# Performance work log

Measured on AMD Instinct MI355X. Metric: run time of the kernel, lower is better.

The kernel has to match this reference:

```python
import jax, jax.numpy as jnp
import numpy as np

B, P, F = 128, 196, 2048   # batch, num_pixels, feature_dim
E, H, V = 512, 512, 10000  # embed_dim, hidden_dim, vocab_size
T = 32                     # max caption length


def setup_inputs() -> dict:
    key = jax.random.key(0)
    ks = jax.random.split(key, 12)
    s_e, s_h, s_f = 1.0 / np.sqrt(E), 1.0 / np.sqrt(H), 1.0 / np.sqrt(F)
    return {
        "features": jax.random.normal(ks[0], (B, P, F), jnp.float32),
        "captions": jax.random.randint(ks[1], (B, T), 0, V),
        # embedding table (init uniform(-0.1, 0.1) in the original)
        "emb_W": jax.random.uniform(ks[2], (V, E), jnp.float32, -0.1, 0.1),
        # LSTMCell params (PyTorch layout: [4H, in] with gate order i,f,g,o)
        "W_ih": jax.random.uniform(ks[3], (4 * H, E), jnp.float32, -s_h, s_h),
        "W_hh": jax.random.uniform(ks[4], (4 * H, H), jnp.float32, -s_h, s_h),
        "b_ih": jax.random.uniform(ks[5], (4 * H,), jnp.float32, -s_h, s_h),
        "b_hh": jax.random.uniform(ks[6], (4 * H,), jnp.float32, -s_h, s_h),
        # init_h / init_c linear layers: feature_dim -> hidden_dim
        "Wh": jax.random.uniform(ks[7], (H, F), jnp.float32, -s_f, s_f),
        "bh": jax.random.uniform(ks[8], (H,), jnp.float32, -s_f, s_f),
        "Wc": jax.random.uniform(ks[9], (H, F), jnp.float32, -s_f, s_f),
        "bc": jax.random.uniform(ks[10], (H,), jnp.float32, -s_f, s_f),
        # output projection (uniform(-0.1, 0.1) weights, zero bias)
        "fc_W": jax.random.uniform(ks[11], (V, H), jnp.float32, -0.1, 0.1),
        "fc_b": jnp.zeros((V,), jnp.float32),
    }


def _decode(features, captions, emb_W, W_ih, W_hh, b_ih, b_hh, Wh, bh, Wc, bc, fc_W, fc_b):
    # init hidden state from mean pooled features
    mean_feat = features.mean(axis=1)                       # [B, F]
    h0 = mean_feat @ Wh.T + bh                              # [B, H]
    c0 = mean_feat @ Wc.T + bc                              # [B, H]

    embeds = emb_W[captions]                                # [B, T, E]
    # x-side gate preactivations for all steps at once: [T-1, B, 4H]
    x_gates = jnp.einsum('bte,ge->tbg', embeds[:, :-1, :], W_ih) + (b_ih + b_hh)

    def step(carry, xg):
        h, c = carry
        gates = xg + h @ W_hh.T                             # [B, 4H]
        i, f, g, o = jnp.split(gates, 4, axis=-1)
        i, f, o = jax.nn.sigmoid(i), jax.nn.sigmoid(f), jax.nn.sigmoid(o)
        g = jnp.tanh(g)
        c_new = f * c + i * g
        h_new = o * jnp.tanh(c_new)
        return (h_new, c_new), h_new

    _, hs = jax.lax.scan(step, (h0, c0), x_gates)           # hs: [T-1, B, H]
    hs = jnp.swapaxes(hs, 0, 1)                             # [B, T-1, H]
    # dropout is identity in eval mode; fc applied per step == batched matmul
    return jnp.einsum('bth,vh->btv', hs, fc_W) + fc_b       # [B, T-1, V]


def reference(features, captions, emb_W, W_ih, W_hh, b_ih, b_hh, Wh, bh, Wc, bc, fc_W, fc_b):
    return _decode(features, captions, emb_W, W_ih, W_hh, b_ih, b_hh, Wh, bh, Wc, bc, fc_W, fc_b)
```

## Files before the change

kernel.cpp:

```cpp
#include <hip/hip_runtime.h>
#include <hip/hip_bf16.h>
#include <cstddef>

#define Bz 128
#define Pz 196
#define Fz 2048
#define Ez 512
#define Hz 512
#define Vz 10000
#define Tz 32
#define TM 31
#define Mrows (Bz * TM)
#define MPAD 4096
#define G4 (4 * Hz)
#define NPAD 10240

typedef __attribute__((ext_vector_type(8))) short bf16x8;
typedef __attribute__((ext_vector_type(4))) float f32x4;

__device__ __forceinline__ void gload_lds16(const void* g, void* l) {
    __builtin_amdgcn_global_load_lds(
        (const __attribute__((address_space(1))) unsigned int*)g,
        (__attribute__((address_space(3))) unsigned int*)l, 16, 0, 0);
}
__device__ __forceinline__ ushort f2b(float x) {
    __hip_bfloat16 b = __float2bfloat16(x);
    return *reinterpret_cast<ushort*>(&b);
}
__device__ __forceinline__ float b2f(ushort u) {
    __hip_bfloat16 b = *reinterpret_cast<__hip_bfloat16*>(&u);
    return __bfloat162float(b);
}

__global__ __launch_bounds__(256) void meanpool(const float* __restrict__ feat,
                                                float* __restrict__ mean) {
    int idx = blockIdx.x * 256 + threadIdx.x;
    int b = idx >> 9;
    int q = idx & 511;
    const float4* base = reinterpret_cast<const float4*>(feat) +
                         (size_t)b * Pz * (Fz / 4) + q;
    float4 acc = {0.f, 0.f, 0.f, 0.f};
    for (int p = 0; p < Pz; ++p) {
        float4 v = base[(size_t)p * (Fz / 4)];
        acc.x += v.x; acc.y += v.y; acc.z += v.z; acc.w += v.w;
    }
    const float s = 1.0f / (float)Pz;
    acc.x *= s; acc.y *= s; acc.z *= s; acc.w *= s;
    reinterpret_cast<float4*>(mean)[idx] = acc;
}

__global__ __launch_bounds__(256) void gather_cvt_emb(const float* __restrict__ emb,
                                                      const int* __restrict__ cap,
                                                      ushort* __restrict__ out) {
    int idx = blockIdx.x * 256 + threadIdx.x;
    if (idx >= Mrows * (Ez / 4)) return;
    int m = idx >> 7, kq = idx & 127;
    int b = m / TM;
    int t = m - b * TM;
    int row = cap[b * Tz + t];
    float4 v = reinterpret_cast<const float4*>(emb + (size_t)row * Ez)[kq];
    ushort4 o = {f2b(v.x), f2b(v.y), f2b(v.z), f2b(v.w)};
    reinterpret_cast<ushort4*>(out + (size_t)m * Ez)[kq] = o;
}

__global__ __launch_bounds__(256) void permute_w(
    const float* __restrict__ Wih, const float* __restrict__ Whh,
    const float* __restrict__ b1,  const float* __restrict__ b2,
    ushort* __restrict__ WihP, ushort* __restrict__ WhhP,
    float* __restrict__ bP) {
    int idx = blockIdx.x * 256 + threadIdx.x;
    int sel = idx >> 18;
    int rem = idx & ((1 << 18) - 1);
    int o = rem >> 7, kq = rem & 127;
    int j = o >> 2, g = o & 3;
    int in = g * Hz + j;
    if (sel == 0) {
        float4 v = reinterpret_cast<const float4*>(Wih + (size_t)in * Ez)[kq];
        ushort4 u = {f2b(v.x), f2b(v.y), f2b(v.z), f2b(v.w)};
        reinterpret_cast<ushort4*>(WihP + (size_t)o * Ez)[kq] = u;
        if (kq == 0) bP[o] = b1[in] + b2[in];
    } else {
        float4 v = reinterpret_cast<const float4*>(Whh + (size_t)in * Hz)[kq];
        ushort4 u = {f2b(v.x), f2b(v.y), f2b(v.z), f2b(v.w)};
        reinterpret_cast<ushort4*>(WhhP + (size_t)o * Hz)[kq] = u;
    }
}

__global__ __launch_bounds__(256) void cvt_bf16_pad4(const float* __restrict__ s,
                                                     ushort* __restrict__ d,
                                                     int n4src, int n4dst) {
    int i = blockIdx.x * 256 + threadIdx.x;
    if (i >= n4dst) return;
    ushort4 o;
    if (i < n4src) {
        float4 v = reinterpret_cast<const float4*>(s)[i];
        o.x = f2b(v.x); o.y = f2b(v.y); o.z = f2b(v.z); o.w = f2b(v.w);
    } else {
        o.x = o.y = o.z = o.w = 0;
    }
    reinterpret_cast<ushort4*>(d)[i] = o;
}

__global__ __launch_bounds__(256) void initk(
    const float* __restrict__ mean,
    const float* __restrict__ Wh, const float* __restrict__ Wc,
    float* __restrict__ partial)
{
    __shared__ float As[64][33];
    __shared__ float Bs2[64][33];
    const int n0 = blockIdx.x * 64;
    const int m0 = blockIdx.y * 64;
    const int kz = blockIdx.z;
    const int tid = threadIdx.x;
    const int tx = tid & 15, ty = tid >> 4;
    float acc[4][4] = {};

    for (int k0 = kz * 256; k0 < kz * 256 + 256; k0 += 32) {
#pragma unroll
        for (int i = 0; i < 2; ++i) {
            int e  = tid + i * 256;
            int r  = e >> 3;
            int cc = (e & 7) << 2;
            float4 va = *reinterpret_cast<const float4*>(
                mean + (size_t)(m0 + r) * Fz + k0 + cc);
            As[r][cc + 0] = va.x; As[r][cc + 1] = va.y;
            As[r][cc + 2] = va.z; As[r][cc + 3] = va.w;
            int n = n0 + r;
            const float* Brow = (n < Hz) ? (Wh + (size_t)n * Fz)
                                         : (Wc + (size_t)(n - Hz) * Fz);
            float4 vb = *reinterpret_cast<const float4*>(Brow + k0 + cc);
            Bs2[r][cc + 0] = vb.x; Bs2[r][cc + 1] = vb.y;
            Bs2[r][cc + 2] = vb.z; Bs2[r][cc + 3] = vb.w;
        }
        __syncthreads();
#pragma unroll
        for (int kk = 0; kk < 32; ++kk) {
            float a[4], bb[4];
#pragma unroll
            for (int i = 0; i < 4; ++i) a[i] = As[ty * 4 + i][kk];
#pragma unroll
            for (int j = 0; j < 4; ++j) bb[j] = Bs2[tx * 4 + j][kk];
#pragma unroll
            for (int i = 0; i < 4; ++i)
#pragma unroll
                for (int j = 0; j < 4; ++j)
                    acc[i][j] += a[i] * bb[j];
        }
        __syncthreads();
    }
#pragma unroll
    for (int i = 0; i < 4; ++i)
#pragma unroll
        for (int j = 0; j < 4; ++j)
            partial[((size_t)kz * 128 + m0 + ty * 4 + i) * 1024 + n0 + tx * 4 + j]
                = acc[i][j];
}

__global__ __launch_bounds__(256) void init_reduce(
    const float* __restrict__ partial,
    const float* __restrict__ bh, const float* __restrict__ bc,
    ushort* __restrict__ haHi, ushort* __restrict__ haLo,
    float* __restrict__ c0f)
{
    int idx = blockIdx.x * 256 + threadIdx.x;
    if (idx >= 128 * 1024) return;
    int m = idx >> 10, n = idx & 1023;
    float s = 0.f;
#pragma unroll
    for (int z = 0; z < 8; ++z)
        s += partial[((size_t)z * 128 + m) * 1024 + n];
    if (n < Hz) {
        s += bh[n];
        ushort hh = f2b(s);
        haHi[(size_t)m * Hz + n] = hh;
        haLo[(size_t)m * Hz + n] = f2b(s - b2f(hh));
    } else {
        c0f[(size_t)m * Hz + (n - Hz)] = s + bc[n - Hz];
    }
}

__global__ __launch_bounds__(256) void gemm_mfma(
    const ushort* __restrict__ A,
    const ushort* __restrict__ B,
    const float* __restrict__ bias,
    float* __restrict__ C,
    int Nb, int ldc, int K)
{
    __shared__ short Al[2][128 * 32];
    __shared__ short Bl[2][128 * 32];
    const int tid  = threadIdx.x;
    const int w    = tid >> 6;
    const int lane = tid & 63;

    const int nwg  = gridDim.x * gridDim.y;
    int orig = blockIdx.y * gridDim.x + blockIdx.x;
    int q = nwg >> 3, r = nwg & 7;
    int xcd = orig & 7, local = orig >> 3;
    int wgid = (xcd < r ? xcd * (q + 1) : r * (q + 1) + (xcd - r) * q) + local;
    const int m0 = (wgid / gridDim.x) * 128;
    const int n0 = (wgid % gridDim.x) * 128;
    const int wr = w >> 1, wc = w & 1;

    f32x4 acc[4][4] = {};

    const int srow = w * 32 + (lane >> 2);
    const int scol = (lane & 3) * 16;
    const char* Ag = (const char*)(A + (size_t)(m0 + srow) * K) + scol;
    const char* Bg = (const char*)(B + (size_t)(n0 + srow) * K) + scol;
    const size_t rstep = (size_t)16 * K * 2;
    const int ldsb = (w * 32) * 32;

    const int ko = (lane >> 4) * 8;
    const int fr = lane & 15;
    const int nk = K >> 5;

    gload_lds16(Ag,         Al[0] + ldsb);
    gload_lds16(Ag + rstep, Al[0] + ldsb + 16 * 32);
    gload_lds16(Bg,         Bl[0] + ldsb);
    gload_lds16(Bg + rstep, Bl[0] + ldsb + 16 * 32);
    __syncthreads();

    int cur = 0;
    for (int k = 0; k < nk; ++k) {
        if (k + 1 < nk) {
            const size_t kb = (size_t)(k + 1) * 64;
            gload_lds16(Ag + kb,         Al[cur ^ 1] + ldsb);
            gload_lds16(Ag + kb + rstep, Al[cur ^ 1] + ldsb + 16 * 32);
            gload_lds16(Bg + kb,         Bl[cur ^ 1] + ldsb);
            gload_lds16(Bg + kb + rstep, Bl[cur ^ 1] + ldsb + 16 * 32);
        }
        bf16x8 af[4], bf[4];
#pragma unroll
        for (int i = 0; i < 4; ++i)
            af[i] = *reinterpret_cast<const bf16x8*>(&Al[cur][(wr * 64 + i * 16 + fr) * 32 + ko]);
#pragma unroll
        for (int j = 0; j < 4; ++j)
            bf[j] = *reinterpret_cast<const bf16x8*>(&Bl[cur][(wc * 64 + j * 16 + fr) * 32 + ko]);
#pragma unroll
        for (int i = 0; i < 4; ++i)
#pragma unroll
            for (int j = 0; j < 4; ++j)
                acc[i][j] = __builtin_amdgcn_mfma_f32_16x16x32_bf16(
                    af[i], bf[j], acc[i][j], 0, 0, 0);
        __syncthreads();
        cur ^= 1;
    }

    const int r0 = (lane >> 4) * 4;
#pragma unroll
    for (int i = 0; i < 4; ++i) {
        int row = m0 + wr * 64 + i * 16 + r0;
#pragma unroll
        for (int j = 0; j < 4; ++j) {
            int col = n0 + wc * 64 + j * 16 + fr;
            if (col < Nb) {
                float bb = bias ? bias[col] : 0.f;
#pragma unroll
                for (int rr = 0; rr < 4; ++rr)
                    C[(size_t)(row + rr) * ldc + col] = acc[i][j][rr] + bb;
            }
        }
    }
}

__global__ __launch_bounds__(512) void fc256(
    const ushort* __restrict__ A,
    const ushort* __restrict__ B,
    const float* __restrict__ bias,
    float* __restrict__ C)
{
    __shared__ short Al[2][256 * 32];
    __shared__ short Bl[2][256 * 32];
    const int tid  = threadIdx.x;
    const int w    = tid >> 6;
    const int lane = tid & 63;

    int orig = blockIdx.x;
    int wgid = (orig & 7) * 80 + (orig >> 3);
    const int m0 = (wgid / 40) * 256;
    const int n0 = (wgid % 40) * 256;
    const int wr = w >> 2, wc = w & 3;

    f32x4 acc[8][4] = {};

    const int srow = w * 32 + (lane >> 2);
    const int scol = (lane & 3) * 16;
    const char* Ag = (const char*)(A + (size_t)(m0 + srow) * Hz) + scol;
    const char* Bg = (const char*)(B + (size_t)(n0 + srow) * Hz) + scol;
    const size_t rstep = (size_t)16 * Hz * 2;
    const int ldsb = (w * 32) * 32;

    const int ko = (lane >> 4) * 8;
    const int fr = lane & 15;

    gload_lds16(Ag,         Al[0] + ldsb);
    gload_lds16(Ag + rstep, Al[0] + ldsb + 16 * 32);
    gload_lds16(Bg,         Bl[0] + ldsb);
    gload_lds16(Bg + rstep, Bl[0] + ldsb + 16 * 32);
    __syncthreads();

    int cur = 0;
#pragma unroll 1
    for (int k = 0; k < 16; ++k) {
        if (k < 15) {
            const size_t kb = (size_t)(k + 1) * 64;
            gload_lds16(Ag + kb,         Al[cur ^ 1] + ldsb);
            gload_lds16(Ag + kb + rstep, Al[cur ^ 1] + ldsb + 16 * 32);
            gload_lds16(Bg + kb,         Bl[cur ^ 1] + ldsb);
            gload_lds16(Bg + kb + rstep, Bl[cur ^ 1] + ldsb + 16 * 32);
        }
        bf16x8 bf[4];
#pragma unroll
        for (int j = 0; j < 4; ++j)
            bf[j] = *reinterpret_cast<const bf16x8*>(&Bl[cur][(wc * 64 + j * 16 + fr) * 32 + ko]);
#pragma unroll
        for (int i = 0; i < 8; ++i) {
            bf16x8 af = *reinterpret_cast<const bf16x8*>(&Al[cur][(wr * 128 + i * 16 + fr) * 32 + ko]);
#pragma unroll
            for (int j = 0; j < 4; ++j)
                acc[i][j] = __builtin_amdgcn_mfma_f32_16x16x32_bf16(
                    af, bf[j], acc[i][j], 0, 0, 0);
        }
        __syncthreads();
        cur ^= 1;
    }

    const int r0 = (lane >> 4) * 4;
#pragma unroll
    for (int i = 0; i < 8; ++i) {
        int row = m0 + wr * 128 + i * 16 + r0;
        if (row >= Mrows) continue;
#pragma unroll
        for (int j = 0; j < 4; ++j) {
            int col = n0 + wc * 64 + j * 16 + fr;
            if (col < Vz) {
                float bb = bias[col];
#pragma unroll
                for (int rr = 0; rr < 4; ++rr)
                    C[(size_t)(row + rr) * Vz + col] = acc[i][j][rr] + bb;
            }
        }
    }
}

__global__ __launch_bounds__(256) void lstm_step3(
    const float* __restrict__ xg,
    const ushort* __restrict__ Whi,
    const ushort* __restrict__ Ah,  const ushort* __restrict__ Alo,
    ushort* __restrict__ Oh, ushort* __restrict__ Ol,
    float* __restrict__ cst, ushort* __restrict__ hsb, int t)
{
    __shared__ float Cl[2][32][33];

    const int tid  = threadIdx.x;
    const int w    = tid >> 6;
    const int kh   = w >> 1;
    const int ch   = w & 1;
    const int lane = tid & 63;
    const int fr   = lane & 15;
    const int hi4  = lane >> 4;
    const int n0   = blockIdx.x * 32;
    const int j0   = blockIdx.x * 8;
    const int m0w  = blockIdx.y * 32;

    const int lm = tid >> 3;
    const int hq = tid & 7;
    const int em = m0w + lm;
    const int ej = j0 + hq;
    const float4 xv = *reinterpret_cast<const float4*>(
        xg + ((size_t)em * TM + t) * G4 + n0 + hq * 4);
    const float cold = cst[(size_t)em * Hz + ej];

    f32x4 acc[2] = {};
    const size_t kbase = (size_t)kh * 256;
    const ushort* Bp  = Whi + (size_t)(n0 + ch * 16 + fr) * Hz + kbase;
    const ushort* Ap0 = Ah  + (size_t)(m0w + fr) * Hz + kbase;
    const ushort* Ap1 = Ah  + (size_t)(m0w + 16 + fr) * Hz + kbase;
    const ushort* Lp0 = Alo + (size_t)(m0w + fr) * Hz + kbase;
    const ushort* Lp1 = Alo + (size_t)(m0w + 16 + fr) * Hz + kbase;

#pragma unroll
    for (int kc = 0; kc < 8; ++kc) {
        const size_t koff = (size_t)kc * 32 + hi4 * 8;
        bf16x8 bv  = *reinterpret_cast<const bf16x8*>(Bp  + koff);
        bf16x8 ah0 = *reinterpret_cast<const bf16x8*>(Ap0 + koff);
        bf16x8 ah1 = *reinterpret_cast<const bf16x8*>(Ap1 + koff);
        bf16x8 al0 = *reinterpret_cast<const bf16x8*>(Lp0 + koff);
        bf16x8 al1 = *reinterpret_cast<const bf16x8*>(Lp1 + koff);
        acc[0] = __builtin_amdgcn_mfma_f32_16x16x32_bf16(ah0, bv, acc[0], 0, 0, 0);
        acc[1] = __builtin_amdgcn_mfma_f32_16x16x32_bf16(ah1, bv, acc[1], 0, 0, 0);
        acc[0] = __builtin_amdgcn_mfma_f32_16x16x32_bf16(al0, bv, acc[0], 0, 0, 0);
        acc[1] = __builtin_amdgcn_mfma_f32_16x16x32_bf16(al1, bv, acc[1], 0, 0, 0);
    }

#pragma unroll
    for (int i = 0; i < 2; ++i)
#pragma unroll
        for (int r = 0; r < 4; ++r)
            Cl[kh][i * 16 + hi4 * 4 + r][ch * 16 + fr] = acc[i][r];
    __syncthreads();

    {
        const int bc = hq * 4;
        float gi = Cl[0][lm][bc + 0] + Cl[1][lm][bc + 0] + xv.x;
        float gf = Cl[0][lm][bc + 1] + Cl[1][lm][bc + 1] + xv.y;
        float gg = Cl[0][lm][bc + 2] + Cl[1][lm][bc + 2] + xv.z;
        float go = Cl[0][lm][bc + 3] + Cl[1][lm][bc + 3] + xv.w;

        float ig = 1.f / (1.f + expf(-gi));
        float fg = 1.f / (1.f + expf(-gf));
        float gt = tanhf(gg);
        float og = 1.f / (1.f + expf(-go));

        float cn = fg * cold + ig * gt;
        float hv = og * tanhf(cn);
        cst[(size_t)em * Hz + ej] = cn;

        ushort hh = f2b(hv);
        ushort hl = f2b(hv - b2f(hh));
        Oh[(size_t)em * Hz + ej] = hh;
        Ol[(size_t)em * Hz + ej] = hl;
        hsb[((size_t)em * TM + t) * Hz + ej] = hh;
    }
}

extern "C" void kernel_launch(void* const* d_in, const int* in_sizes, int n_in,
                              void* d_out, int out_size, void* d_ws, size_t ws_size,
                              hipStream_t stream) {
    const float* features = (const float*)d_in[0];
    const int*   captions = (const int*)d_in[1];
    const float* emb_W    = (const float*)d_in[2];
    const float* W_ih     = (const float*)d_in[3];
    const float* W_hh     = (const float*)d_in[4];
    const float* b_ih     = (const float*)d_in[5];
    const float* b_hh     = (const float*)d_in[6];
    const float* Wh       = (const float*)d_in[7];
    const float* bh       = (const float*)d_in[8];
    const float* Wc       = (const float*)d_in[9];
    const float* bc       = (const float*)d_in[10];
    const float* fc_W     = (const float*)d_in[11];
    const float* fc_b     = (const float*)d_in[12];
    float* out = (float*)d_out;

    float* w    = (float*)d_ws;
    float* mean = w;
    float* xg   = mean + Bz * Fz;
    float* partial = xg;
    float* c0f  = xg + (size_t)Mrows * G4;
    float* bP   = c0f + Bz * Hz;
    ushort* embg = (ushort*)(bP + G4);
    ushort* WihP = embg + (size_t)Mrows * Ez;
    ushort* Whi  = WihP + (size_t)G4 * Ez;
    ushort* fcWb = Whi + (size_t)G4 * Hz;
    ushort* hsb  = fcWb + (size_t)NPAD * Hz;
    ushort* haHi = hsb + (size_t)MPAD * Hz;
    ushort* haLo = haHi + Bz * Hz;
    ushort* hbHi = haLo + Bz * Hz;
    ushort* hbLo = hbHi + Bz * Hz;

    meanpool<<<(Bz * Fz / 4) / 256, 256, 0, stream>>>(features, mean);
    gather_cvt_emb<<<(Mrows * (Ez / 4) + 255) / 256, 256, 0, stream>>>(emb_W, captions, embg);
    permute_w<<<(2 * G4 * (Hz / 4)) / 256, 256, 0, stream>>>(
        W_ih, W_hh, b_ih, b_hh, WihP, Whi, bP);
    cvt_bf16_pad4<<<(NPAD * Hz / 4 + 255) / 256, 256, 0, stream>>>(
        fc_W, fcWb, Vz * Hz / 4, NPAD * Hz / 4);

    initk<<<dim3(16, 2, 8), 256, 0, stream>>>(mean, Wh, Wc, partial);
    init_reduce<<<(128 * 1024) / 256, 256, 0, stream>>>(
        partial, bh, bc, haHi, haLo, c0f);

    gemm_mfma<<<dim3(G4 / 128, Mrows / 128), 256, 0, stream>>>(
        embg, WihP, bP, xg, G4, G4, Ez);

    for (int t = 0; t < TM; ++t) {
        const ushort* ih = (t & 1) ? hbHi : haHi;
        const ushort* il = (t & 1) ? hbLo : haLo;
        ushort* oh = (t & 1) ? haHi : hbHi;
        ushort* ol = (t & 1) ? haLo : hbLo;
        lstm_step3<<<dim3(64, 4), 256, 0, stream>>>(
            xg, Whi, ih, il, oh, ol, c0f, hsb, t);
    }

    fc256<<<640, 512, 0, stream>>>(hsb, fcWb, fc_b, out);
}
```

Baseline: 436.7 us.

## Deepen FC GEMM pipeline to four LDS stages with swizzled layout

Rewrites the output-projection GEMM main loop to use a 4-buffer LDS ring with three stages of global-to-LDS loads in flight, using explicit vmcnt waits instead of a full __syncthreads per iteration. It also XOR-swizzles the LDS layout to reduce bank conflicts on fragment reads, preloads all A/B fragments before the MFMA block, and raises wave priority during MFMAs. This is meant to hide global memory latency and LDS conflicts better, at the cost of 128KB of LDS, which limits occupancy to one block per CU.

```diff
diff --git a/kernel.cpp b/kernel.cpp
--- a/kernel.cpp
+++ b/kernel.cpp
@@ -263,17 +263,18 @@
     }
 }
 
-__global__ __launch_bounds__(512) void fc256(
+__global__ __launch_bounds__(512) void fc8(
     const ushort* __restrict__ A,
     const ushort* __restrict__ B,
     const float* __restrict__ bias,
     float* __restrict__ C)
 {
-    __shared__ short Al[2][256 * 32];
-    __shared__ short Bl[2][256 * 32];
+    __shared__ short Lds[4][2][256 * 32];
+
     const int tid  = threadIdx.x;
     const int w    = tid >> 6;
     const int lane = tid & 63;
+    const int fr   = lane & 15;
 
     int orig = blockIdx.x;
     int wgid = (orig & 7) * 80 + (orig >> 3);
@@ -283,47 +284,69 @@
 
     f32x4 acc[8][4] = {};
 
-    const int srow = w * 32 + (lane >> 2);
-    const int scol = (lane & 3) * 16;
-    const char* Ag = (const char*)(A + (size_t)(m0 + srow) * Hz) + scol;
-    const char* Bg = (const char*)(B + (size_t)(n0 + srow) * Hz) + scol;
-    const size_t rstep = (size_t)16 * Hz * 2;
-    const int ldsb = (w * 32) * 32;
-
-    const int ko = (lane >> 4) * 8;
-    const int fr = lane & 15;
-
-    gload_lds16(Ag,         Al[0] + ldsb);
-    gload_lds16(Ag + rstep, Al[0] + ldsb + 16 * 32);
-    gload_lds16(Bg,         Bl[0] + ldsb);
-    gload_lds16(Bg + rstep, Bl[0] + ldsb + 16 * 32);
-    __syncthreads();
-
-    int cur = 0;
+    const int sw16 = (((lane & 3) ^ ((lane >> 3) & 3)) << 4);
+    const int srowA = lane >> 2;
+
+    const int rsw = (((lane >> 4) ^ ((fr >> 1) & 3)) << 4);
+
+#define FC_STAGE(T_) do {                                                     \
+    const int b_ = (T_) & 3;                                                  \
+    const size_t kb_ = (size_t)(T_) * 64;                                     \
+    _Pragma("unroll")                                                         \
+    for (int q_ = 0; q_ < 2; ++q_) {                                          \
+        const int R_ = w * 32 + q_ * 16;                                      \
+        gload_lds16((const char*)A + (size_t)(m0 + R_ + srowA) * 1024 + kb_ + sw16, \
+                    (char*)&Lds[b_][0][0] + R_ * 64);                         \
+        gload_lds16((const char*)B + (size_t)(n0 + R_ + srowA) * 1024 + kb_ + sw16, \
+                    (char*)&Lds[b_][1][0] + R_ * 64);                         \
+    }                                                                         \
+} while (0)
+
+#define FC_ITER(K_, VM_) do {                                                 \
+    if ((K_) + 3 <= 15) FC_STAGE((K_) + 3);                                   \
+    asm volatile("s_waitcnt vmcnt(" #VM_ ")" ::: "memory");                   \
+    __builtin_amdgcn_s_barrier();                                             \
+    __builtin_amdgcn_sched_barrier(0);                                        \
+    const int b_ = (K_) & 3;                                                  \
+    const char* Ab_ = (const char*)&Lds[b_][0][0];                            \
+    const char* Bb_ = (const char*)&Lds[b_][1][0];                            \
+    bf16x8 bfr_[4];                                                           \
+    _Pragma("unroll")                                                         \
+    for (int j_ = 0; j_ < 4; ++j_)                                            \
+        bfr_[j_] = *reinterpret_cast<const bf16x8*>(                          \
+            Bb_ + (wc * 64 + j_ * 16 + fr) * 64 + rsw);                       \
+    bf16x8 afr_[8];                                                           \
+    _Pragma("unroll")                                                         \
+    for (int i_ = 0; i_ < 8; ++i_)                                            \
+        afr_[i_] = *reinterpret_cast<const bf16x8*>(                          \
+            Ab_ + (wr * 128 + i_ * 16 + fr) * 64 + rsw);                      \
+    asm volatile("s_waitcnt lgkmcnt(0)" ::: "memory");                        \
+    __builtin_amdgcn_sched_barrier(0);                                        \
+    __builtin_amdgcn_s_barrier();                                             \
+    __builtin_amdgcn_s_setprio(1);                                            \
+    _Pragma("unroll")                                                         \
+    for (int i_ = 0; i_ < 8; ++i_)                                            \
+        _Pragma("unroll")                                                     \
+        for (int j_ = 0; j_ < 4; ++j_)                                        \
+            acc[i_][j_] = __builtin_amdgcn_mfma_f32_16x16x32_bf16(            \
+                afr_[i_], bfr_[j_], acc[i_][j_], 0, 0, 0);                    \
+    __builtin_amdgcn_s_setprio(0);                                            \
+} while (0)
+
+    FC_STAGE(0);
+    FC_STAGE(1);
+    FC_STAGE(2);
+
 #pragma unroll 1
-    for (int k = 0; k < 16; ++k) {
-        if (k < 15) {
-            const size_t kb = (size_t)(k + 1) * 64;
-            gload_lds16(Ag + kb,         Al[cur ^ 1] + ldsb);
-            gload_lds16(Ag + kb + rstep, Al[cur ^ 1] + ldsb + 16 * 32);
-            gload_lds16(Bg + kb,         Bl[cur ^ 1] + ldsb);
-            gload_lds16(Bg + kb + rstep, Bl[cur ^ 1] + ldsb + 16 * 32);
-        }
-        bf16x8 bf[4];
-#pragma unroll
-        for (int j = 0; j < 4; ++j)
-            bf[j] = *reinterpret_cast<const bf16x8*>(&Bl[cur][(wc * 64 + j * 16 + fr) * 32 + ko]);
-#pragma unroll
-        for (int i = 0; i < 8; ++i) {
-            bf16x8 af = *reinterpret_cast<const bf16x8*>(&Al[cur][(wr * 128 + i * 16 + fr) * 32 + ko]);
-#pragma unroll
-            for (int j = 0; j < 4; ++j)
-                acc[i][j] = __builtin_amdgcn_mfma_f32_16x16x32_bf16(
-                    af, bf[j], acc[i][j], 0, 0, 0);
-        }
-        __syncthreads();
-        cur ^= 1;
-    }
+    for (int k = 0; k <= 12; ++k) {
+        FC_ITER(k, 12);
+    }
+    FC_ITER(13, 8);
+    FC_ITER(14, 4);
+    FC_ITER(15, 0);
+
+#undef FC_STAGE
+#undef FC_ITER
 
     const int r0 = (lane >> 4) * 4;
 #pragma unroll
@@ -481,5 +504,5 @@
             xg, Whi, ih, il, oh, ol, c0f, hsb, t);
     }
 
-    fc256<<<640, 512, 0, stream>>>(hsb, fcWb, fc_b, out);
-}
+    fc8<<<640, 512, 0, stream>>>(hsb, fcWb, fc_b, out);
+}
```

Result: no change. 428.9 us (-1.8%).

## Overlap FC projection of previous step with LSTM recurrence in fused kernel

Applied to the files above, without the earlier changes.

Removes the separate large fc256 GEMM and instead has each per-timestep launch carry 64 extra blocks that compute the vocabulary projection for the previous step's hidden states. The launch loop runs one extra iteration to finish the last step. This aims to fill idle CUs during the latency-bound recurrence with the output GEMM. In exchange the FC work loses LDS tiling and reads fc_W directly from global memory every step, which puts more bandwidth pressure on the recurrent critical path.

```diff
diff --git a/kernel.cpp b/kernel.cpp
--- a/kernel.cpp
+++ b/kernel.cpp
@@ -263,105 +263,73 @@
     }
 }
 
-__global__ __launch_bounds__(512) void fc256(
-    const ushort* __restrict__ A,
-    const ushort* __restrict__ B,
-    const float* __restrict__ bias,
-    float* __restrict__ C)
-{
-    __shared__ short Al[2][256 * 32];
-    __shared__ short Bl[2][256 * 32];
-    const int tid  = threadIdx.x;
-    const int w    = tid >> 6;
-    const int lane = tid & 63;
-
-    int orig = blockIdx.x;
-    int wgid = (orig & 7) * 80 + (orig >> 3);
-    const int m0 = (wgid / 40) * 256;
-    const int n0 = (wgid % 40) * 256;
-    const int wr = w >> 2, wc = w & 3;
-
-    f32x4 acc[8][4] = {};
-
-    const int srow = w * 32 + (lane >> 2);
-    const int scol = (lane & 3) * 16;
-    const char* Ag = (const char*)(A + (size_t)(m0 + srow) * Hz) + scol;
-    const char* Bg = (const char*)(B + (size_t)(n0 + srow) * Hz) + scol;
-    const size_t rstep = (size_t)16 * Hz * 2;
-    const int ldsb = (w * 32) * 32;
-
-    const int ko = (lane >> 4) * 8;
-    const int fr = lane & 15;
-
-    gload_lds16(Ag,         Al[0] + ldsb);
-    gload_lds16(Ag + rstep, Al[0] + ldsb + 16 * 32);
-    gload_lds16(Bg,         Bl[0] + ldsb);
-    gload_lds16(Bg + rstep, Bl[0] + ldsb + 16 * 32);
-    __syncthreads();
-
-    int cur = 0;
-#pragma unroll 1
-    for (int k = 0; k < 16; ++k) {
-        if (k < 15) {
-            const size_t kb = (size_t)(k + 1) * 64;
-            gload_lds16(Ag + kb,         Al[cur ^ 1] + ldsb);
-            gload_lds16(Ag + kb + rstep, Al[cur ^ 1] + ldsb + 16 * 32);
-            gload_lds16(Bg + kb,         Bl[cur ^ 1] + ldsb);
-            gload_lds16(Bg + kb + rstep, Bl[cur ^ 1] + ldsb + 16 * 32);
-        }
-        bf16x8 bf[4];
-#pragma unroll
-        for (int j = 0; j < 4; ++j)
-            bf[j] = *reinterpret_cast<const bf16x8*>(&Bl[cur][(wc * 64 + j * 16 + fr) * 32 + ko]);
-#pragma unroll
-        for (int i = 0; i < 8; ++i) {
-            bf16x8 af = *reinterpret_cast<const bf16x8*>(&Al[cur][(wr * 128 + i * 16 + fr) * 32 + ko]);
-#pragma unroll
-            for (int j = 0; j < 4; ++j)
-                acc[i][j] = __builtin_amdgcn_mfma_f32_16x16x32_bf16(
-                    af, bf[j], acc[i][j], 0, 0, 0);
-        }
-        __syncthreads();
-        cur ^= 1;
-    }
-
-    const int r0 = (lane >> 4) * 4;
-#pragma unroll
-    for (int i = 0; i < 8; ++i) {
-        int row = m0 + wr * 128 + i * 16 + r0;
-        if (row >= Mrows) continue;
-#pragma unroll
-        for (int j = 0; j < 4; ++j) {
-            int col = n0 + wc * 64 + j * 16 + fr;
-            if (col < Vz) {
-                float bb = bias[col];
-#pragma unroll
-                for (int rr = 0; rr < 4; ++rr)
-                    C[(size_t)(row + rr) * Vz + col] = acc[i][j][rr] + bb;
-            }
-        }
-    }
-}
-
-__global__ __launch_bounds__(256) void lstm_step3(
+__global__ __launch_bounds__(256) void lstm_fused(
     const float* __restrict__ xg,
     const ushort* __restrict__ Whi,
     const ushort* __restrict__ Ah,  const ushort* __restrict__ Alo,
     ushort* __restrict__ Oh, ushort* __restrict__ Ol,
-    float* __restrict__ cst, ushort* __restrict__ hsb, int t)
+    float* __restrict__ cst, ushort* __restrict__ hsb,
+    const ushort* __restrict__ fcWb, const float* __restrict__ fc_b,
+    float* __restrict__ out, int t)
 {
-    __shared__ float Cl[2][32][33];
-
+    const int beta = blockIdx.x;
     const int tid  = threadIdx.x;
-    const int w    = tid >> 6;
-    const int kh   = w >> 1;
-    const int ch   = w & 1;
+    const int wv   = tid >> 6;
     const int lane = tid & 63;
     const int fr   = lane & 15;
     const int hi4  = lane >> 4;
-    const int n0   = blockIdx.x * 32;
-    const int j0   = blockIdx.x * 8;
-    const int m0w  = blockIdx.y * 32;
+
+    if (beta >= 256) {
+        if (t < 1) return;
+        const int f   = beta - 256;
+        const int n0  = f * 160;
+        const int tm1 = t - 1;
+        const int b0  = wv * 32;
+
+        f32x4 acc[2][10] = {};
+        const ushort* A0 = hsb + ((size_t)(b0 + fr) * TM + tm1) * Hz;
+        const ushort* A1 = hsb + ((size_t)(b0 + 16 + fr) * TM + tm1) * Hz;
+#pragma unroll
+        for (int kc = 0; kc < 16; ++kc) {
+            const size_t koff = (size_t)kc * 32 + hi4 * 8;
+            bf16x8 a0 = *reinterpret_cast<const bf16x8*>(A0 + koff);
+            bf16x8 a1 = *reinterpret_cast<const bf16x8*>(A1 + koff);
+#pragma unroll
+            for (int nf = 0; nf < 10; ++nf) {
+                bf16x8 bv = *reinterpret_cast<const bf16x8*>(
+                    fcWb + (size_t)(n0 + nf * 16 + fr) * Hz + koff);
+                acc[0][nf] = __builtin_amdgcn_mfma_f32_16x16x32_bf16(a0, bv, acc[0][nf], 0, 0, 0);
+                acc[1][nf] = __builtin_amdgcn_mfma_f32_16x16x32_bf16(a1, bv, acc[1][nf], 0, 0, 0);
+            }
+        }
+        const int r0 = hi4 * 4;
+#pragma unroll
+        for (int mi = 0; mi < 2; ++mi) {
+#pragma unroll
+            for (int nf = 0; nf < 10; ++nf) {
+                int col = n0 + nf * 16 + fr;
+                if (col >= Vz) continue;
+                float bb = fc_b[col];
+#pragma unroll
+                for (int rr = 0; rr < 4; ++rr) {
+                    int b = b0 + mi * 16 + r0 + rr;
+                    out[((size_t)b * TM + tm1) * Vz + col] = acc[mi][nf][rr] + bb;
+                }
+            }
+        }
+        return;
+    }
+
+    if (t >= TM) return;
+    __shared__ float Cl[2][32][33];
+
+    const int cg  = beta & 63;
+    const int mq  = beta >> 6;
+    const int kh  = wv >> 1;
+    const int ch  = wv & 1;
+    const int n0  = cg * 32;
+    const int j0  = cg * 8;
+    const int m0w = mq * 32;
 
     const int lm = tid >> 3;
     const int hq = tid & 7;
@@ -472,14 +440,12 @@
     gemm_mfma<<<dim3(G4 / 128, Mrows / 128), 256, 0, stream>>>(
         embg, WihP, bP, xg, G4, G4, Ez);
 
-    for (int t = 0; t < TM; ++t) {
+    for (int t = 0; t <= TM; ++t) {
         const ushort* ih = (t & 1) ? hbHi : haHi;
         const ushort* il = (t & 1) ? hbLo : haLo;
         ushort* oh = (t & 1) ? haHi : hbHi;
         ushort* ol = (t & 1) ? haLo : hbLo;
-        lstm_step3<<<dim3(64, 4), 256, 0, stream>>>(
-            xg, Whi, ih, il, oh, ol, c0f, hsb, t);
-    }
-
-    fc256<<<640, 512, 0, stream>>>(hsb, fcWb, fc_b, out);
-}
+        lstm_fused<<<320, 256, 0, stream>>>(
+            xg, Whi, ih, il, oh, ol, c0f, hsb, fcWb, fc_b, out, t);
+    }
+}
```

After: 1.187 ms. +171.7%, slower.
